# Kernel optimization log

Hardware: AMD Instinct MI355X
Metric: run time of the kernel (lower is better)

## Reference

```python
import jax, jax.numpy as jnp
import numpy as np

B, S, D = 2, 2048, 768
C = 8                # num_channels
R = D // C           # ternary_rank = 96 (RoPE head_dim)
THETA = 10000.0
TERNARY_STD = 0.2
TERNARY_SCALE = 1.0  # ternary_factor_scaling


def _rope_tables():
    # HF-style RoPE: inv_freq over half dim, emb = concat(freqs, freqs)
    inv_freq = 1.0 / (THETA ** (np.arange(0, R, 2, dtype=np.float32) / R))
    pos = np.arange(S, dtype=np.float32)
    freqs = pos[:, None] * inv_freq[None, :]          # [S, R/2]
    emb = np.concatenate([freqs, freqs], axis=-1)     # [S, R]
    cos = np.broadcast_to(np.cos(emb)[None], (B, S, R)).copy()
    sin = np.broadcast_to(np.sin(emb)[None], (B, S, R)).copy()
    return jnp.asarray(cos), jnp.asarray(sin)


def setup_inputs() -> dict:
    key = jax.random.key(0)
    k1, k2, k3 = jax.random.split(key, 3)
    qz = jax.random.normal(k1, (B, S, D), dtype=jnp.float32)
    U = jax.random.normal(k2, (D, D), dtype=jnp.float32) * TERNARY_STD
    V = jax.random.normal(k3, (D, D), dtype=jnp.float32) * TERNARY_STD
    cos, sin = _rope_tables()
    return {"qz": qz, "cos": cos, "sin": sin, "U": U, "V": V}


def _rotate_half(x):
    h = x.shape[-1] // 2
    return jnp.concatenate([-x[..., h:], x[..., :h]], axis=-1)


def reference(qz, cos, sin, U, V):
    # cos/sin: [B,S,R] -> broadcast over channel dim -> [B,1,S,R]
    cosb = cos[:, None, :, :]
    sinb = sin[:, None, :, :]
    rope = lambda x: x * cosb + _rotate_half(x) * sinb       # apply
    rope_o = lambda x: x * cosb - _rotate_half(x) * sinb     # apply_o (inverse)

    # projections: F.linear(qz, W) == qz @ W.T
    qz_u = (qz @ U.T * TERNARY_SCALE).reshape(B, S, C, R).transpose(0, 2, 1, 3)
    qz_v = (qz @ V.T * TERNARY_SCALE).reshape(B, S, C, R).transpose(0, 2, 1, 3)

    qz_uo = rope_o(qz_u)
    qz_ur = rope(qz_u)
    qz_vr = rope(qz_v)

    # message_F: [B,C,S,S]
    message_F = jnp.einsum('bcqr,bckr->bcqk', qz_ur, qz_vr)
    # softmax(message_F / regularize_h) with regularize_h = 1/D  ->  * D
    qh = jax.nn.softmax((message_F * jnp.float32(D)).astype(jnp.float32), axis=-1).astype(qz_ur.dtype)

    qh_v1 = rope_o(jnp.einsum('bcqk,bckr->bcqr', qh, qz_vr))  # qh @ qz_v
    qh_v2 = rope(jnp.einsum('bckq,bckr->bcqr', qh, qz_uo))    # qh^T @ qz_uo

    qh_v1 = qh_v1.transpose(0, 2, 1, 3).reshape(B, S, D)
    qh_v2 = qh_v2.transpose(0, 2, 1, 3).reshape(B, S, D)

    message_G = (qh_v1 @ U + qh_v2 @ V) * TERNARY_SCALE
    return message_G
```

## Files before the change

### kernel.cpp

```cpp
#include <hip/hip_runtime.h>

typedef _Float16 f16;
typedef _Float16 f16x8 __attribute__((ext_vector_type(8)));
typedef _Float16 f16x4 __attribute__((ext_vector_type(4)));
typedef float f32x4 __attribute__((ext_vector_type(4)));

#define MFMA16(A,B,C) __builtin_amdgcn_mfma_f32_16x16x32_f16(A,B,C,0,0,0)
#define INV2048 4.8828125e-4f
#define HN (16ll*2048*96)
#define UVN 589824
#define ZC1 1107.98979f
#define ZC2 0.54101064f

__device__ __forceinline__ void split_f16(float x, f16& h, f16& l) {
    h = (f16)x;
    l = (f16)((x - (float)h) * 2048.0f);
}

__global__ __launch_bounds__(256) void k0_split(const float* __restrict__ qz,
                                                const float* __restrict__ U,
                                                const float* __restrict__ V,
                                                f16* __restrict__ qzh, f16* __restrict__ qzl,
                                                f16* __restrict__ Uh, f16* __restrict__ Ul,
                                                f16* __restrict__ Vh, f16* __restrict__ Vl) {
    const int i4 = blockIdx.x * 256 + threadIdx.x;
    {
        float4 x = *(const float4*)(qz + (size_t)i4 * 4);
        f16 h0, l0, h1, l1, h2, l2, h3, l3;
        split_f16(x.x, h0, l0); split_f16(x.y, h1, l1);
        split_f16(x.z, h2, l2); split_f16(x.w, h3, l3);
        f16x4 hv = {h0, h1, h2, h3};
        f16x4 lv = {l0, l1, l2, l3};
        *(f16x4*)(qzh + (size_t)i4 * 4) = hv;
        *(f16x4*)(qzl + (size_t)i4 * 4) = lv;
    }
    if (i4 < UVN / 4) {
        float4 x = *(const float4*)(U + (size_t)i4 * 4);
        f16 h0, l0, h1, l1, h2, l2, h3, l3;
        split_f16(x.x, h0, l0); split_f16(x.y, h1, l1);
        split_f16(x.z, h2, l2); split_f16(x.w, h3, l3);
        f16x4 hv = {h0, h1, h2, h3};
        f16x4 lv = {l0, l1, l2, l3};
        *(f16x4*)(Uh + (size_t)i4 * 4) = hv;
        *(f16x4*)(Ul + (size_t)i4 * 4) = lv;
        float4 y = *(const float4*)(V + (size_t)i4 * 4);
        split_f16(y.x, h0, l0); split_f16(y.y, h1, l1);
        split_f16(y.z, h2, l2); split_f16(y.w, h3, l3);
        f16x4 hv2 = {h0, h1, h2, h3};
        f16x4 lv2 = {l0, l1, l2, l3};
        *(f16x4*)(Vh + (size_t)i4 * 4) = hv2;
        *(f16x4*)(Vl + (size_t)i4 * 4) = lv2;
    }
}

__global__ __launch_bounds__(256, 2) void k1_proj(const f16* __restrict__ qzh,
                                                  const f16* __restrict__ qzl,
                                                  const f16* __restrict__ Uh,
                                                  const f16* __restrict__ Ul,
                                                  const f16* __restrict__ Vh,
                                                  const f16* __restrict__ Vl,
                                                  const float* __restrict__ cosb,
                                                  const float* __restrict__ sinb,
                                                  f16* __restrict__ uhp, f16* __restrict__ ulp,
                                                  f16* __restrict__ vhp, f16* __restrict__ vlp,
                                                  f16* __restrict__ vT, f16* __restrict__ oT) {
    __shared__ __align__(16) f16 smem[36864];
    f16* sAh  = smem;
    f16* sAl  = smem + 4608;
    f16* sBuh = smem + 9216;
    f16* sBul = smem + 9216 + 6912;
    f16* sBvh = smem + 9216 + 2 * 6912;
    f16* sBvl = smem + 9216 + 3 * 6912;

    const int tid = threadIdx.x;
    const int w = tid >> 6, lane = tid & 63;
    const int quad = lane >> 4, l15 = lane & 15;
    const int wr = w >> 1, wc = w & 1;
    const int bid0 = blockIdx.y * 64 + blockIdx.x;
    const int swz  = (bid0 & 7) * 64 + (bid0 >> 3);
    const int bs0 = (swz & 63) * 64;
    const int c = swz >> 6;

    const f16* Ug_h = Uh + (size_t)c * 96 * 768;
    const f16* Ug_l = Ul + (size_t)c * 96 * 768;
    const f16* Vg_h = Vh + (size_t)c * 96 * 768;
    const f16* Vg_l = Vl + (size_t)c * 96 * 768;

    f32x4 aUS[2][3] = {}, aUX[2][3] = {};
    f32x4 aVS[2][3] = {}, aVX[2][3] = {};

    for (int k0 = 0; k0 < 768; k0 += 64) {
        __syncthreads();
#pragma unroll
        for (int m = 0; m < 2; ++m) {
            int f = tid + 256 * m, row = f >> 3, cg = f & 7;
            const size_t go = (size_t)(bs0 + row) * 768 + k0 + cg * 8;
            const int lo = row * 72 + cg * 8;
            *(float4*)&sAh[lo] = *(const float4*)(qzh + go);
            *(float4*)&sAl[lo] = *(const float4*)(qzl + go);
        }
#pragma unroll
        for (int m = 0; m < 3; ++m) {
            int f = tid + 256 * m, row = f >> 3, cg = f & 7;
            const size_t go = (size_t)row * 768 + k0 + cg * 8;
            const int lo = row * 72 + cg * 8;
            *(float4*)&sBuh[lo] = *(const float4*)(Ug_h + go);
            *(float4*)&sBul[lo] = *(const float4*)(Ug_l + go);
            *(float4*)&sBvh[lo] = *(const float4*)(Vg_h + go);
            *(float4*)&sBvl[lo] = *(const float4*)(Vg_l + go);
        }
        __syncthreads();
#pragma unroll
        for (int cc = 0; cc < 2; ++cc) {
            f16x8 ah[2], al[2];
#pragma unroll
            for (int mt = 0; mt < 2; ++mt) {
                const int ar = (32 * wr + 16 * mt + l15) * 72 + cc * 32 + quad * 8;
                ah[mt] = *(const f16x8*)&sAh[ar];
                al[mt] = *(const f16x8*)&sAl[ar];
            }
#pragma unroll
            for (int nt = 0; nt < 3; ++nt) {
                const int br = (48 * wc + 16 * nt + l15) * 72 + cc * 32 + quad * 8;
                f16x8 buh = *(const f16x8*)&sBuh[br];
                f16x8 bul = *(const f16x8*)&sBul[br];
                f16x8 bvh = *(const f16x8*)&sBvh[br];
                f16x8 bvl = *(const f16x8*)&sBvl[br];
#pragma unroll
                for (int mt = 0; mt < 2; ++mt) {
                    aUS[mt][nt] = MFMA16(ah[mt], buh, aUS[mt][nt]);
                    aUX[mt][nt] = MFMA16(ah[mt], bul, aUX[mt][nt]);
                    aUX[mt][nt] = MFMA16(al[mt], buh, aUX[mt][nt]);
                    aVS[mt][nt] = MFMA16(ah[mt], bvh, aVS[mt][nt]);
                    aVX[mt][nt] = MFMA16(ah[mt], bvl, aVX[mt][nt]);
                    aVX[mt][nt] = MFMA16(al[mt], bvh, aVX[mt][nt]);
                }
            }
        }
    }

    __syncthreads();
    float* LU = (float*)smem;
    float* LV = LU + 6400;
#pragma unroll
    for (int mt = 0; mt < 2; ++mt)
#pragma unroll
        for (int nt = 0; nt < 3; ++nt)
#pragma unroll
            for (int r = 0; r < 4; ++r) {
                const int sl = 32 * wr + 16 * mt + 4 * quad + r;
                const int col = 48 * wc + 16 * nt + l15;
                LU[sl * 100 + col] = aUS[mt][nt][r] + aUX[mt][nt][r] * INV2048;
                LV[sl * 100 + col] = aVS[mt][nt][r] + aVX[mt][nt][r] * INV2048;
            }
    __syncthreads();

    const int b = bs0 >> 11;
    const int s0 = bs0 & 2047;
    const int head = b * 8 + c;
    const size_t nb = (size_t)head * 2048 * 96;
    const size_t tb = (size_t)head * 96 * 2048;
    const int ty = tid >> 4, tx = tid & 15;

#pragma unroll
    for (int jj = 0; jj < 3; ++jj) {
        int r = tx + 16 * jj;
        f16 vt1[4], vt2[4], ot1[4], ot2[4];
#pragma unroll
        for (int ii = 0; ii < 4; ++ii) {
            int sl = 4 * ty + ii;
            int s = s0 + sl;
            int cbi = (b * 2048 + s) * 96 + r;
            float cc = cosb[cbi], ss = sinb[cbi];
            size_t rowb = nb + (size_t)s * 96;
            float u1 = LU[sl * 100 + r], u2 = LU[sl * 100 + r + 48];
            float v1 = LV[sl * 100 + r], v2 = LV[sl * 100 + r + 48];
            float ur1 = u1 * cc - u2 * ss, ur2 = u2 * cc + u1 * ss;
            float uo1 = u1 * cc + u2 * ss, uo2 = u2 * cc - u1 * ss;
            float vr1 = v1 * cc - v2 * ss, vr2 = v2 * cc + v1 * ss;
            f16 h, l;
            split_f16(ur1, h, l); uhp[rowb + r] = h;      ulp[rowb + r] = l;
            split_f16(ur2, h, l); uhp[rowb + r + 48] = h; ulp[rowb + r + 48] = l;
            split_f16(vr1, h, l); vhp[rowb + r] = h;      vlp[rowb + r] = l;      vt1[ii] = h;
            split_f16(vr2, h, l); vhp[rowb + r + 48] = h; vlp[rowb + r + 48] = l; vt2[ii] = h;
            ot1[ii] = (f16)uo1; ot2[ii] = (f16)uo2;
        }
        f16x4 pv1 = {vt1[0], vt1[1], vt1[2], vt1[3]};
        f16x4 pv2 = {vt2[0], vt2[1], vt2[2], vt2[3]};
        f16x4 po1 = {ot1[0], ot1[1], ot1[2], ot1[3]};
        f16x4 po2 = {ot2[0], ot2[1], ot2[2], ot2[3]};
        *(f16x4*)&vT[tb + (size_t)r * 2048 + s0 + 4 * ty] = pv1;
        *(f16x4*)&vT[tb + (size_t)(r + 48) * 2048 + s0 + 4 * ty] = pv2;
        *(f16x4*)&oT[tb + (size_t)r * 2048 + s0 + 4 * ty] = po1;
        *(f16x4*)&oT[tb + (size_t)(r + 48) * 2048 + s0 + 4 * ty] = po2;
    }
}

__global__ __launch_bounds__(256, 2) void k2_stats(const f16* __restrict__ uhp,
                                                   const f16* __restrict__ ulp,
                                                   const f16* __restrict__ vhp,
                                                   const f16* __restrict__ vlp,
                                                   float* __restrict__ Mo) {
    __shared__ float Mbuf[4][64];
    const int tid = threadIdx.x, w = tid >> 6, lane = tid & 63;
    const int quad = lane >> 4, l15 = lane & 15;
    const int bid0 = blockIdx.y * 32 + blockIdx.x;
    const int swz  = (bid0 & 7) * 64 + (bid0 >> 3);
    const int q0 = (swz & 31) * 64, head = swz >> 5;
    const f16* Ah_g = uhp + (size_t)head * 2048 * 96;
    const f16* Al_g = ulp + (size_t)head * 2048 * 96;

    f16x8 Afh[4][3], Afl[4][3];
#pragma unroll
    for (int mt = 0; mt < 4; ++mt)
#pragma unroll
        for (int cc = 0; cc < 3; ++cc) {
            size_t off = (size_t)(q0 + 16 * mt + l15) * 96 + cc * 32 + quad * 8;
            Afh[mt][cc] = *(const f16x8*)(Ah_g + off);
            Afl[mt][cc] = *(const f16x8*)(Al_g + off);
        }

    const f16* Bh_p = vhp + (size_t)head * 2048 * 96 + (size_t)(w * 16 + l15) * 96 + quad * 8;
    const f16* Bl_p = vlp + (size_t)head * 2048 * 96 + (size_t)(w * 16 + l15) * 96 + quad * 8;

    f16x8 Bch[2][3], Bcl[2][3];
#pragma unroll
    for (int cc = 0; cc < 3; ++cc) {
        Bch[0][cc] = *(const f16x8*)(Bh_p + cc * 32);
        Bcl[0][cc] = *(const f16x8*)(Bl_p + cc * 32);
    }

    float m_run[4][4];
#pragma unroll
    for (int mt = 0; mt < 4; ++mt)
#pragma unroll
        for (int r = 0; r < 4; ++r) m_run[mt][r] = -3.0e38f;

    for (int tp = 0; tp < 16; ++tp) {
#pragma unroll
        for (int h = 0; h < 2; ++h) {
            const int t = 2 * tp + h;
            if (t < 31) {
                const f16* bh = Bh_p + (size_t)(t + 1) * 6144;
                const f16* bl = Bl_p + (size_t)(t + 1) * 6144;
#pragma unroll
                for (int cc = 0; cc < 3; ++cc) {
                    Bch[h ^ 1][cc] = *(const f16x8*)(bh + cc * 32);
                    Bcl[h ^ 1][cc] = *(const f16x8*)(bl + cc * 32);
                }
            }
            f32x4 accS[4] = {}, accX[4] = {};
            __builtin_amdgcn_s_setprio(1);
#pragma unroll
            for (int cc = 0; cc < 3; ++cc)
#pragma unroll
                for (int mt = 0; mt < 4; ++mt) {
                    accS[mt] = MFMA16(Afh[mt][cc], Bch[h][cc], accS[mt]);
                    accX[mt] = MFMA16(Afh[mt][cc], Bcl[h][cc], accX[mt]);
                    accX[mt] = MFMA16(Afl[mt][cc], Bch[h][cc], accX[mt]);
                }
            __builtin_amdgcn_s_setprio(0);
#pragma unroll
            for (int mt = 0; mt < 4; ++mt)
#pragma unroll
                for (int r = 0; r < 4; ++r) {
                    float zl = fmaf(ZC1, accS[mt][r], ZC2 * accX[mt][r]);
                    m_run[mt][r] = fmaxf(m_run[mt][r], zl);
                }
        }
    }
#pragma unroll
    for (int mt = 0; mt < 4; ++mt)
#pragma unroll
        for (int r = 0; r < 4; ++r) {
            float m = m_run[mt][r];
            m = fmaxf(m, __shfl_xor(m, 1)); m = fmaxf(m, __shfl_xor(m, 2));
            m = fmaxf(m, __shfl_xor(m, 4)); m = fmaxf(m, __shfl_xor(m, 8));
            m_run[mt][r] = m;
        }
    if (l15 == 0) {
#pragma unroll
        for (int mt = 0; mt < 4; ++mt)
#pragma unroll
            for (int r = 0; r < 4; ++r)
                Mbuf[w][16 * mt + 4 * quad + r] = m_run[mt][r];
    }
    __syncthreads();
    if (tid < 64) {
        float M = -3.0e38f;
#pragma unroll
        for (int ww = 0; ww < 4; ++ww) M = fmaxf(M, Mbuf[ww][tid]);
        Mo[head * 2048 + q0 + tid] = M;
    }
}

__global__ __launch_bounds__(256, 2) void k3a(const f16* __restrict__ uhp,
                                              const f16* __restrict__ ulp,
                                              const f16* __restrict__ vhp,
                                              const f16* __restrict__ vlp,
                                              const f16* __restrict__ vT,
                                              const float* __restrict__ Mo,
                                              float* __restrict__ Lo,
                                              const float* __restrict__ cosb,
                                              const float* __restrict__ sinb,
                                              f16* __restrict__ w1) {
    __shared__ f16 Vt[2][112 * 72];
    __shared__ f16 P[2][64 * 72];
    const int tid = threadIdx.x, w = tid >> 6, lane = tid & 63;
    const int quad = lane >> 4, l15 = lane & 15;
    const int bid0 = blockIdx.y * 32 + blockIdx.x;
    const int swz  = (bid0 & 7) * 64 + (bid0 >> 3);
    const int q0 = (swz & 31) * 64, head = swz >> 5;
    const f16* Ah_g = uhp + (size_t)head * 2048 * 96;
    const f16* Al_g = ulp + (size_t)head * 2048 * 96;
    const f16* Vt_g = vT + (size_t)head * 96 * 2048;

    f16x8 Afh[4][3], Afl[4][3];
#pragma unroll
    for (int mt = 0; mt < 4; ++mt)
#pragma unroll
        for (int cc = 0; cc < 3; ++cc) {
            size_t off = (size_t)(q0 + 16 * mt + l15) * 96 + cc * 32 + quad * 8;
            Afh[mt][cc] = *(const f16x8*)(Ah_g + off);
            Afl[mt][cc] = *(const f16x8*)(Al_g + off);
        }
    float negM[4][4];
#pragma unroll
    for (int mt = 0; mt < 4; ++mt)
#pragma unroll
        for (int r = 0; r < 4; ++r)
            negM[mt][r] = -Mo[head * 2048 + q0 + 16 * mt + 4 * quad + r];

    const f16* Bh_p = vhp + (size_t)head * 2048 * 96 + (size_t)(w * 16 + l15) * 96 + quad * 8;
    const f16* Bl_p = vlp + (size_t)head * 2048 * 96 + (size_t)(w * 16 + l15) * 96 + quad * 8;
    const int vr0 = tid >> 3, vc8 = (tid & 7) * 8;
    const int pwc = (w * 16 + l15 + 16 * quad) & 63;
    const int prr = 16 * (l15 >> 2);

    if (tid < 144) {
        f16x8 ones = {(f16)1, (f16)1, (f16)1, (f16)1,
                      (f16)1, (f16)1, (f16)1, (f16)1};
        *(f16x8*)&Vt[0][96 * 72 + tid * 8] = ones;
        *(f16x8*)&Vt[1][96 * 72 + tid * 8] = ones;
    }

    f16x8 Bch[2][3], Bcl[2][3];
    float4 v0, v1, v2;
#pragma unroll
    for (int cc = 0; cc < 3; ++cc) {
        Bch[0][cc] = *(const f16x8*)(Bh_p + cc * 32);
        Bcl[0][cc] = *(const f16x8*)(Bl_p + cc * 32);
    }
    v0 = *(const float4*)(Vt_g + (size_t)vr0 * 2048 + vc8);
    v1 = *(const float4*)(Vt_g + (size_t)(vr0 + 32) * 2048 + vc8);
    v2 = *(const float4*)(Vt_g + (size_t)(vr0 + 64) * 2048 + vc8);
    *(float4*)&Vt[0][vr0 * 72 + vc8] = v0;
    *(float4*)&Vt[0][(vr0 + 32) * 72 + vc8] = v1;
    *(float4*)&Vt[0][(vr0 + 64) * 72 + vc8] = v2;

    f32x4 accO[7] = {};

    for (int tp = 0; tp < 16; ++tp) {
#pragma unroll
        for (int h = 0; h < 2; ++h) {
            const int t = 2 * tp + h;
            if (t < 31) {
                const f16* bh = Bh_p + (size_t)(t + 1) * 6144;
                const f16* bl = Bl_p + (size_t)(t + 1) * 6144;
                const int kn = (t + 1) * 64;
#pragma unroll
                for (int cc = 0; cc < 3; ++cc) {
                    Bch[h ^ 1][cc] = *(const f16x8*)(bh + cc * 32);
                    Bcl[h ^ 1][cc] = *(const f16x8*)(bl + cc * 32);
                }
                v0 = *(const float4*)(Vt_g + (size_t)vr0 * 2048 + kn + vc8);
                v1 = *(const float4*)(Vt_g + (size_t)(vr0 + 32) * 2048 + kn + vc8);
                v2 = *(const float4*)(Vt_g + (size_t)(vr0 + 64) * 2048 + kn + vc8);
            }
            f32x4 accS[4] = {}, accX[4] = {};
            __builtin_amdgcn_s_setprio(1);
#pragma unroll
            for (int cc = 0; cc < 3; ++cc)
#pragma unroll
                for (int mt = 0; mt < 4; ++mt) {
                    accS[mt] = MFMA16(Afh[mt][cc], Bch[h][cc], accS[mt]);
                    accX[mt] = MFMA16(Afh[mt][cc], Bcl[h][cc], accX[mt]);
                    accX[mt] = MFMA16(Afl[mt][cc], Bch[h][cc], accX[mt]);
                }
            __builtin_amdgcn_s_setprio(0);
#pragma unroll
            for (int mt = 0; mt < 4; ++mt)
#pragma unroll
                for (int r = 0; r < 4; ++r) {
                    float zl = fmaf(ZC1, accS[mt][r], ZC2 * accX[mt][r]);
                    P[h][(16 * mt + 4 * quad + r) * 72 + pwc] =
                        (f16)exp2f(zl + negM[mt][r]);
                }
            __syncthreads();
            __builtin_amdgcn_s_setprio(1);
#pragma unroll
            for (int kc = 0; kc < 2; ++kc) {
                f16x8 ap = *(const f16x8*)&P[h][(w * 16 + l15) * 72 +
                                               ((kc * 32 + quad * 8 + prr) & 63)];
#pragma unroll
                for (int nt = 0; nt < 7; ++nt) {
                    f16x8 bv = *(const f16x8*)&Vt[h][(nt * 16 + l15) * 72 + kc * 32 + quad * 8];
                    accO[nt] = MFMA16(ap, bv, accO[nt]);
                }
            }
            __builtin_amdgcn_s_setprio(0);
            if (t < 31) {
                *(float4*)&Vt[h ^ 1][vr0 * 72 + vc8] = v0;
                *(float4*)&Vt[h ^ 1][(vr0 + 32) * 72 + vc8] = v1;
                *(float4*)&Vt[h ^ 1][(vr0 + 64) * 72 + vc8] = v2;
            }
        }
    }
    float invL[4];
#pragma unroll
    for (int r = 0; r < 4; ++r) invL[r] = 1.0f / accO[6][r];
    if (l15 == 0) {
#pragma unroll
        for (int r = 0; r < 4; ++r)
            Lo[head * 2048 + q0 + w * 16 + quad * 4 + r] = accO[6][r];
    }

    const int b = head >> 3, c = head & 7;
#pragma unroll
    for (int r = 0; r < 4; ++r) {
        int q = q0 + w * 16 + quad * 4 + r;
        int cbi = (b * 2048 + q) * 96;
        f16* wrow = w1 + (size_t)(b * 2048 + q) * 768 + c * 96;
#pragma unroll
        for (int nt = 0; nt < 3; ++nt) {
            int rr = nt * 16 + l15;
            float cc = cosb[cbi + rr], ss = sinb[cbi + rr];
            float a = accO[nt][r] * invL[r];
            float b2 = accO[nt + 3][r] * invL[r];
            wrow[rr] = (f16)(a * cc + b2 * ss);
            wrow[rr + 48] = (f16)(b2 * cc - a * ss);
        }
    }
}

__global__ __launch_bounds__(256, 2) void k3b(const f16* __restrict__ uhp,
                                              const f16* __restrict__ ulp,
                                              const f16* __restrict__ vhp,
                                              const f16* __restrict__ vlp,
                                              const f16* __restrict__ oT,
                                              const float* __restrict__ Mo,
                                              const float* __restrict__ Lo,
                                              const float* __restrict__ cosb,
                                              const float* __restrict__ sinb,
                                              f16* __restrict__ w2) {
    __shared__ f16 Ot[2][96 * 72];
    __shared__ f16 P[2][64 * 72];
    const int tid = threadIdx.x, w = tid >> 6, lane = tid & 63;
    const int quad = lane >> 4, l15 = lane & 15;
    const int bid0 = blockIdx.y * 32 + blockIdx.x;
    const int swz  = (bid0 & 7) * 64 + (bid0 >> 3);
    const int q0 = (swz & 31) * 64, head = swz >> 5;
    const f16* Ah_g = vhp + (size_t)head * 2048 * 96;
    const f16* Al_g = vlp + (size_t)head * 2048 * 96;
    const f16* Ot_g = oT + (size_t)head * 96 * 2048;

    f16x8 Afh[4][3], Afl[4][3];
#pragma unroll
    for (int mt = 0; mt < 4; ++mt)
#pragma unroll
        for (int cc = 0; cc < 3; ++cc) {
            size_t off = (size_t)(q0 + 16 * mt + l15) * 96 + cc * 32 + quad * 8;
            Afh[mt][cc] = *(const f16x8*)(Ah_g + off);
            Afl[mt][cc] = *(const f16x8*)(Al_g + off);
        }

    const f16* Bh_p = uhp + (size_t)head * 2048 * 96 + (size_t)(w * 16 + l15) * 96 + quad * 8;
    const f16* Bl_p = ulp + (size_t)head * 2048 * 96 + (size_t)(w * 16 + l15) * 96 + quad * 8;
    const int vr0 = tid >> 3, vc8 = (tid & 7) * 8;
    const int pwc = (w * 16 + l15 + 16 * quad) & 63;
    const int prr = 16 * (l15 >> 2);

    f16x8 Bch[2][3], Bcl[2][3];
    float4 v0, v1, v2;
#pragma unroll
    for (int cc = 0; cc < 3; ++cc) {
        Bch[0][cc] = *(const f16x8*)(Bh_p + cc * 32);
        Bcl[0][cc] = *(const f16x8*)(Bl_p + cc * 32);
    }
    v0 = *(const float4*)(Ot_g + (size_t)vr0 * 2048 + vc8);
    v1 = *(const float4*)(Ot_g + (size_t)(vr0 + 32) * 2048 + vc8);
    v2 = *(const float4*)(Ot_g + (size_t)(vr0 + 64) * 2048 + vc8);
    *(float4*)&Ot[0][vr0 * 72 + vc8] = v0;
    *(float4*)&Ot[0][(vr0 + 32) * 72 + vc8] = v1;
    *(float4*)&Ot[0][(vr0 + 64) * 72 + vc8] = v2;

    f32x4 accO[6] = {};

    for (int tp = 0; tp < 16; ++tp) {
#pragma unroll
        for (int h = 0; h < 2; ++h) {
            const int t = 2 * tp + h;
            const int k0 = t * 64;
            float negMk = -Mo[head * 2048 + k0 + w * 16 + l15];
            float invLk = 1.0f / Lo[head * 2048 + k0 + w * 16 + l15];
            if (t < 31) {
                const f16* bh = Bh_p + (size_t)(t + 1) * 6144;
                const f16* bl = Bl_p + (size_t)(t + 1) * 6144;
                const int kn = (t + 1) * 64;
#pragma unroll
                for (int cc = 0; cc < 3; ++cc) {
                    Bch[h ^ 1][cc] = *(const f16x8*)(bh + cc * 32);
                    Bcl[h ^ 1][cc] = *(const f16x8*)(bl + cc * 32);
                }
                v0 = *(const float4*)(Ot_g + (size_t)vr0 * 2048 + kn + vc8);
                v1 = *(const float4*)(Ot_g + (size_t)(vr0 + 32) * 2048 + kn + vc8);
                v2 = *(const float4*)(Ot_g + (size_t)(vr0 + 64) * 2048 + kn + vc8);
            }
            f32x4 accS[4] = {}, accX[4] = {};
            __builtin_amdgcn_s_setprio(1);
#pragma unroll
            for (int cc = 0; cc < 3; ++cc)
#pragma unroll
                for (int mt = 0; mt < 4; ++mt) {
                    accS[mt] = MFMA16(Afh[mt][cc], Bch[h][cc], accS[mt]);
                    accX[mt] = MFMA16(Afl[mt][cc], Bch[h][cc], accX[mt]);
                    accX[mt] = MFMA16(Afh[mt][cc], Bcl[h][cc], accX[mt]);
                }
            __builtin_amdgcn_s_setprio(0);
#pragma unroll
            for (int mt = 0; mt < 4; ++mt)
#pragma unroll
                for (int r = 0; r < 4; ++r) {
                    float zl = fmaf(ZC1, accS[mt][r], ZC2 * accX[mt][r]);
                    P[h][(16 * mt + 4 * quad + r) * 72 + pwc] =
                        (f16)(exp2f(zl + negMk) * invLk);
                }
            __syncthreads();
            __builtin_amdgcn_s_setprio(1);
#pragma unroll
            for (int kc = 0; kc < 2; ++kc) {
                f16x8 ap = *(const f16x8*)&P[h][(w * 16 + l15) * 72 +
                                               ((kc * 32 + quad * 8 + prr) & 63)];
#pragma unroll
                for (int nt = 0; nt < 6; ++nt) {
                    f16x8 bo = *(const f16x8*)&Ot[h][(nt * 16 + l15) * 72 + kc * 32 + quad * 8];
                    accO[nt] = MFMA16(ap, bo, accO[nt]);
                }
            }
            __builtin_amdgcn_s_setprio(0);
            if (t < 31) {
                *(float4*)&Ot[h ^ 1][vr0 * 72 + vc8] = v0;
                *(float4*)&Ot[h ^ 1][(vr0 + 32) * 72 + vc8] = v1;
                *(float4*)&Ot[h ^ 1][(vr0 + 64) * 72 + vc8] = v2;
            }
        }
    }
    const int b = head >> 3, c = head & 7;
#pragma unroll
    for (int r = 0; r < 4; ++r) {
        int q = q0 + w * 16 + quad * 4 + r;
        int cbi = (b * 2048 + q) * 96;
        f16* wrow = w2 + (size_t)(b * 2048 + q) * 768 + c * 96;
#pragma unroll
        for (int nt = 0; nt < 3; ++nt) {
            int rr = nt * 16 + l15;
            float cc = cosb[cbi + rr], ss = sinb[cbi + rr];
            float a = accO[nt][r];
            float b2 = accO[nt + 3][r];
            wrow[rr] = (f16)(a * cc - b2 * ss);
            wrow[rr + 48] = (f16)(b2 * cc + a * ss);
        }
    }
}

__global__ __launch_bounds__(256, 2) void k4_final(const f16* __restrict__ w1,
                                                   const f16* __restrict__ w2,
                                                   const float* __restrict__ U,
                                                   const float* __restrict__ V,
                                                   float* __restrict__ outp) {
    __shared__ f16 A1[128 * 56];
    __shared__ f16 A2[128 * 56];
    __shared__ f16 B1[64 * 56];
    __shared__ f16 B2[64 * 56];
    const int tid = threadIdx.x, w = tid >> 6, lane = tid & 63;
    const int quad = lane >> 4, l15 = lane & 15;
    const int bs0 = blockIdx.x * 128;
    const int d0 = blockIdx.y * 64;
    f32x4 acc[2][4] = {};

    for (int ec = 0; ec < 24; ++ec) {
        int e0 = ec * 32;
        __syncthreads();
#pragma unroll
        for (int m = 0; m < 2; ++m) {
            int f = tid + 256 * m;
            int row = f >> 2, q = f & 3;
            *(float4*)&A1[row * 56 + q * 8] =
                *(const float4*)(w1 + (size_t)(bs0 + row) * 768 + e0 + q * 8);
            *(float4*)&A2[row * 56 + q * 8] =
                *(const float4*)(w2 + (size_t)(bs0 + row) * 768 + e0 + q * 8);
        }
#pragma unroll
        for (int m2 = 0; m2 < 2; ++m2) {
            int e_r = (tid >> 4) + 16 * m2;
            int dc = tid & 15;
            float4 fu = *(const float4*)(U + (size_t)(e0 + e_r) * 768 + d0 + dc * 4);
            float4 fv = *(const float4*)(V + (size_t)(e0 + e_r) * 768 + d0 + dc * 4);
            B1[(dc * 4 + 0) * 56 + e_r] = (f16)fu.x;
            B1[(dc * 4 + 1) * 56 + e_r] = (f16)fu.y;
            B1[(dc * 4 + 2) * 56 + e_r] = (f16)fu.z;
            B1[(dc * 4 + 3) * 56 + e_r] = (f16)fu.w;
            B2[(dc * 4 + 0) * 56 + e_r] = (f16)fv.x;
            B2[(dc * 4 + 1) * 56 + e_r] = (f16)fv.y;
            B2[(dc * 4 + 2) * 56 + e_r] = (f16)fv.z;
            B2[(dc * 4 + 3) * 56 + e_r] = (f16)fv.w;
        }
        __syncthreads();
        f16x8 a1f[2], a2f[2];
#pragma unroll
        for (int mt = 0; mt < 2; ++mt) {
            a1f[mt] = *(const f16x8*)&A1[(32 * w + 16 * mt + l15) * 56 + quad * 8];
            a2f[mt] = *(const f16x8*)&A2[(32 * w + 16 * mt + l15) * 56 + quad * 8];
        }
#pragma unroll
        for (int nt = 0; nt < 4; ++nt) {
            f16x8 b1f = *(const f16x8*)&B1[(nt * 16 + l15) * 56 + quad * 8];
            f16x8 b2f = *(const f16x8*)&B2[(nt * 16 + l15) * 56 + quad * 8];
#pragma unroll
            for (int mt = 0; mt < 2; ++mt) {
                acc[mt][nt] = MFMA16(a1f[mt], b1f, acc[mt][nt]);
                acc[mt][nt] = MFMA16(a2f[mt], b2f, acc[mt][nt]);
            }
        }
    }
#pragma unroll
    for (int mt = 0; mt < 2; ++mt)
#pragma unroll
        for (int nt = 0; nt < 4; ++nt)
#pragma unroll
            for (int r = 0; r < 4; ++r) {
                int s = bs0 + 32 * w + 16 * mt + 4 * quad + r;
                int d = d0 + 16 * nt + l15;
                outp[(size_t)s * 768 + d] = acc[mt][nt][r];
            }
}

extern "C" void kernel_launch(void* const* d_in, const int* in_sizes, int n_in,
                              void* d_out, int out_size, void* d_ws, size_t ws_size,
                              hipStream_t stream) {
    const float* qz   = (const float*)d_in[0];
    const float* cosb = (const float*)d_in[1];
    const float* sinb = (const float*)d_in[2];
    const float* U    = (const float*)d_in[3];
    const float* V    = (const float*)d_in[4];
    float* outp = (float*)d_out;

    f16* ws16 = (f16*)d_ws;
    f16* uhp = ws16;
    f16* ulp = ws16 + HN;
    f16* vhp = ws16 + 2 * HN;
    f16* vlp = ws16 + 3 * HN;
    f16* vT  = ws16 + 4 * HN;
    f16* oT  = ws16 + 5 * HN;
    f16* w1  = ws16 + 6 * HN;
    f16* w2  = ws16 + 7 * HN;
    float* Mo = (float*)(ws16 + 8 * HN);
    float* Lo = Mo + 16 * 2048;

    f16* qzh = w1;
    f16* qzl = w2;
    f16* outw = (f16*)d_out;
    f16* Uh = outw;
    f16* Ul = outw + UVN;
    f16* Vh = outw + 2 * UVN;
    f16* Vl = outw + 3 * UVN;

    k0_split<<<dim3(3072), 256, 0, stream>>>(qz, U, V, qzh, qzl, Uh, Ul, Vh, Vl);
    k1_proj<<<dim3(64, 8), 256, 0, stream>>>(qzh, qzl, Uh, Ul, Vh, Vl, cosb, sinb,
                                             uhp, ulp, vhp, vlp, vT, oT);
    k2_stats<<<dim3(32, 16), 256, 0, stream>>>(uhp, ulp, vhp, vlp, Mo);
    k3a<<<dim3(32, 16), 256, 0, stream>>>(uhp, ulp, vhp, vlp, vT, Mo, Lo, cosb, sinb, w1);
    k3b<<<dim3(32, 16), 256, 0, stream>>>(uhp, ulp, vhp, vlp, oT, Mo, Lo, cosb, sinb, w2);
    k4_final<<<dim3(32, 12), 256, 0, stream>>>(w1, w2, U, V, outp);
}
```

Measured before the change: 326.3 us.

## Halve query tile per block and split PV output columns across wave pairs

```diff
diff --git a/kernel.cpp b/kernel.cpp
--- a/kernel.cpp
+++ b/kernel.cpp
@@ -196,23 +196,23 @@
     }
 }
 
-__global__ __launch_bounds__(256, 2) void k2_stats(const f16* __restrict__ uhp,
+__global__ __launch_bounds__(256, 3) void k2_stats(const f16* __restrict__ uhp,
                                                    const f16* __restrict__ ulp,
                                                    const f16* __restrict__ vhp,
                                                    const f16* __restrict__ vlp,
                                                    float* __restrict__ Mo) {
-    __shared__ float Mbuf[4][64];
+    __shared__ float Mbuf[4][32];
     const int tid = threadIdx.x, w = tid >> 6, lane = tid & 63;
     const int quad = lane >> 4, l15 = lane & 15;
-    const int bid0 = blockIdx.y * 32 + blockIdx.x;
-    const int swz  = (bid0 & 7) * 64 + (bid0 >> 3);
-    const int q0 = (swz & 31) * 64, head = swz >> 5;
+    const int bid0 = blockIdx.y * 64 + blockIdx.x;
+    const int swz  = (bid0 & 7) * 128 + (bid0 >> 3);
+    const int q0 = (swz & 63) * 32, head = swz >> 6;
     const f16* Ah_g = uhp + (size_t)head * 2048 * 96;
     const f16* Al_g = ulp + (size_t)head * 2048 * 96;
 
-    f16x8 Afh[4][3], Afl[4][3];
-#pragma unroll
-    for (int mt = 0; mt < 4; ++mt)
+    f16x8 Afh[2][3], Afl[2][3];
+#pragma unroll
+    for (int mt = 0; mt < 2; ++mt)
 #pragma unroll
         for (int cc = 0; cc < 3; ++cc) {
             size_t off = (size_t)(q0 + 16 * mt + l15) * 96 + cc * 32 + quad * 8;
@@ -230,9 +230,9 @@
         Bcl[0][cc] = *(const f16x8*)(Bl_p + cc * 32);
     }
 
-    float m_run[4][4];
-#pragma unroll
-    for (int mt = 0; mt < 4; ++mt)
+    float m_run[2][4];
+#pragma unroll
+    for (int mt = 0; mt < 2; ++mt)
 #pragma unroll
         for (int r = 0; r < 4; ++r) m_run[mt][r] = -3.0e38f;
 
@@ -249,19 +249,19 @@
                     Bcl[h ^ 1][cc] = *(const f16x8*)(bl + cc * 32);
                 }
             }
-            f32x4 accS[4] = {}, accX[4] = {};
+            f32x4 accS[2] = {}, accX[2] = {};
             __builtin_amdgcn_s_setprio(1);
 #pragma unroll
             for (int cc = 0; cc < 3; ++cc)
 #pragma unroll
-                for (int mt = 0; mt < 4; ++mt) {
+                for (int mt = 0; mt < 2; ++mt) {
                     accS[mt] = MFMA16(Afh[mt][cc], Bch[h][cc], accS[mt]);
                     accX[mt] = MFMA16(Afh[mt][cc], Bcl[h][cc], accX[mt]);
                     accX[mt] = MFMA16(Afl[mt][cc], Bch[h][cc], accX[mt]);
                 }
             __builtin_amdgcn_s_setprio(0);
 #pragma unroll
-            for (int mt = 0; mt < 4; ++mt)
+            for (int mt = 0; mt < 2; ++mt)
 #pragma unroll
                 for (int r = 0; r < 4; ++r) {
                     float zl = fmaf(ZC1, accS[mt][r], ZC2 * accX[mt][r]);
@@ -270,7 +270,7 @@
         }
     }
 #pragma unroll
-    for (int mt = 0; mt < 4; ++mt)
+    for (int mt = 0; mt < 2; ++mt)
 #pragma unroll
         for (int r = 0; r < 4; ++r) {
             float m = m_run[mt][r];
@@ -280,13 +280,13 @@
         }
     if (l15 == 0) {
 #pragma unroll
-        for (int mt = 0; mt < 4; ++mt)
+        for (int mt = 0; mt < 2; ++mt)
 #pragma unroll
             for (int r = 0; r < 4; ++r)
                 Mbuf[w][16 * mt + 4 * quad + r] = m_run[mt][r];
     }
     __syncthreads();
-    if (tid < 64) {
+    if (tid < 32) {
         float M = -3.0e38f;
 #pragma unroll
         for (int ww = 0; ww < 4; ++ww) M = fmaxf(M, Mbuf[ww][tid]);
@@ -294,7 +294,7 @@
     }
 }
 
-__global__ __launch_bounds__(256, 2) void k3a(const f16* __restrict__ uhp,
+__global__ __launch_bounds__(256, 3) void k3a(const f16* __restrict__ uhp,
                                               const f16* __restrict__ ulp,
                                               const f16* __restrict__ vhp,
                                               const f16* __restrict__ vlp,
@@ -305,28 +305,30 @@
                                               const float* __restrict__ sinb,
                                               f16* __restrict__ w1) {
     __shared__ f16 Vt[2][112 * 72];
-    __shared__ f16 P[2][64 * 72];
+    __shared__ f16 P[2][32 * 72];
+    __shared__ float Lbuf[32];
     const int tid = threadIdx.x, w = tid >> 6, lane = tid & 63;
     const int quad = lane >> 4, l15 = lane & 15;
-    const int bid0 = blockIdx.y * 32 + blockIdx.x;
-    const int swz  = (bid0 & 7) * 64 + (bid0 >> 3);
-    const int q0 = (swz & 31) * 64, head = swz >> 5;
+    const int qg = w & 1;
+    const int bid0 = blockIdx.y * 64 + blockIdx.x;
+    const int swz  = (bid0 & 7) * 128 + (bid0 >> 3);
+    const int q0 = (swz & 63) * 32, head = swz >> 6;
     const f16* Ah_g = uhp + (size_t)head * 2048 * 96;
     const f16* Al_g = ulp + (size_t)head * 2048 * 96;
     const f16* Vt_g = vT + (size_t)head * 96 * 2048;
 
-    f16x8 Afh[4][3], Afl[4][3];
-#pragma unroll
-    for (int mt = 0; mt < 4; ++mt)
+    f16x8 Afh[2][3], Afl[2][3];
+#pragma unroll
+    for (int mt = 0; mt < 2; ++mt)
 #pragma unroll
         for (int cc = 0; cc < 3; ++cc) {
             size_t off = (size_t)(q0 + 16 * mt + l15) * 96 + cc * 32 + quad * 8;
             Afh[mt][cc] = *(const f16x8*)(Ah_g + off);
             Afl[mt][cc] = *(const f16x8*)(Al_g + off);
         }
-    float negM[4][4];
-#pragma unroll
-    for (int mt = 0; mt < 4; ++mt)
+    float negM[2][4];
+#pragma unroll
+    for (int mt = 0; mt < 2; ++mt)
 #pragma unroll
         for (int r = 0; r < 4; ++r)
             negM[mt][r] = -Mo[head * 2048 + q0 + 16 * mt + 4 * quad + r];
@@ -358,7 +360,7 @@
     *(float4*)&Vt[0][(vr0 + 32) * 72 + vc8] = v1;
     *(float4*)&Vt[0][(vr0 + 64) * 72 + vc8] = v2;
 
-    f32x4 accO[7] = {};
+    f32x4 accO[4] = {};
 
     for (int tp = 0; tp < 16; ++tp) {
 #pragma unroll
@@ -377,19 +379,19 @@
                 v1 = *(const float4*)(Vt_g + (size_t)(vr0 + 32) * 2048 + kn + vc8);
                 v2 = *(const float4*)(Vt_g + (size_t)(vr0 + 64) * 2048 + kn + vc8);
             }
-            f32x4 accS[4] = {}, accX[4] = {};
+            f32x4 accS[2] = {}, accX[2] = {};
             __builtin_amdgcn_s_setprio(1);
 #pragma unroll
             for (int cc = 0; cc < 3; ++cc)
 #pragma unroll
-                for (int mt = 0; mt < 4; ++mt) {
+                for (int mt = 0; mt < 2; ++mt) {
                     accS[mt] = MFMA16(Afh[mt][cc], Bch[h][cc], accS[mt]);
                     accX[mt] = MFMA16(Afh[mt][cc], Bcl[h][cc], accX[mt]);
                     accX[mt] = MFMA16(Afl[mt][cc], Bch[h][cc], accX[mt]);
                 }
             __builtin_amdgcn_s_setprio(0);
 #pragma unroll
-            for (int mt = 0; mt < 4; ++mt)
+            for (int mt = 0; mt < 2; ++mt)
 #pragma unroll
                 for (int r = 0; r < 4; ++r) {
                     float zl = fmaf(ZC1, accS[mt][r], ZC2 * accX[mt][r]);
@@ -400,12 +402,22 @@
             __builtin_amdgcn_s_setprio(1);
 #pragma unroll
             for (int kc = 0; kc < 2; ++kc) {
-                f16x8 ap = *(const f16x8*)&P[h][(w * 16 + l15) * 72 +
+                f16x8 ap = *(const f16x8*)&P[h][(qg * 16 + l15) * 72 +
                                                ((kc * 32 + quad * 8 + prr) & 63)];
-#pragma unroll
-                for (int nt = 0; nt < 7; ++nt) {
-                    f16x8 bv = *(const f16x8*)&Vt[h][(nt * 16 + l15) * 72 + kc * 32 + quad * 8];
-                    accO[nt] = MFMA16(ap, bv, accO[nt]);
+                if (w < 2) {
+                    const int nts[4] = {0, 1, 3, 4};
+#pragma unroll
+                    for (int j = 0; j < 4; ++j) {
+                        f16x8 bv = *(const f16x8*)&Vt[h][(nts[j] * 16 + l15) * 72 + kc * 32 + quad * 8];
+                        accO[j] = MFMA16(ap, bv, accO[j]);
+                    }
+                } else {
+                    const int nts[3] = {2, 5, 6};
+#pragma unroll
+                    for (int j = 0; j < 3; ++j) {
+                        f16x8 bv = *(const f16x8*)&Vt[h][(nts[j] * 16 + l15) * 72 + kc * 32 + quad * 8];
+                        accO[j] = MFMA16(ap, bv, accO[j]);
+                    }
                 }
             }
             __builtin_amdgcn_s_setprio(0);
@@ -416,34 +428,46 @@
             }
         }
     }
+    if (w >= 2 && l15 == 0) {
+#pragma unroll
+        for (int r = 0; r < 4; ++r) {
+            Lbuf[qg * 16 + 4 * quad + r] = accO[2][r];
+            Lo[head * 2048 + q0 + qg * 16 + 4 * quad + r] = accO[2][r];
+        }
+    }
+    __syncthreads();
     float invL[4];
 #pragma unroll
-    for (int r = 0; r < 4; ++r) invL[r] = 1.0f / accO[6][r];
-    if (l15 == 0) {
-#pragma unroll
-        for (int r = 0; r < 4; ++r)
-            Lo[head * 2048 + q0 + w * 16 + quad * 4 + r] = accO[6][r];
-    }
+    for (int r = 0; r < 4; ++r) invL[r] = 1.0f / Lbuf[qg * 16 + 4 * quad + r];
 
     const int b = head >> 3, c = head & 7;
 #pragma unroll
     for (int r = 0; r < 4; ++r) {
-        int q = q0 + w * 16 + quad * 4 + r;
+        int q = q0 + qg * 16 + quad * 4 + r;
         int cbi = (b * 2048 + q) * 96;
         f16* wrow = w1 + (size_t)(b * 2048 + q) * 768 + c * 96;
-#pragma unroll
-        for (int nt = 0; nt < 3; ++nt) {
-            int rr = nt * 16 + l15;
+        if (w < 2) {
+#pragma unroll
+            for (int p = 0; p < 2; ++p) {
+                int rr = p * 16 + l15;
+                float cc = cosb[cbi + rr], ss = sinb[cbi + rr];
+                float a = accO[p][r] * invL[r];
+                float b2 = accO[p + 2][r] * invL[r];
+                wrow[rr] = (f16)(a * cc + b2 * ss);
+                wrow[rr + 48] = (f16)(b2 * cc - a * ss);
+            }
+        } else {
+            int rr = 32 + l15;
             float cc = cosb[cbi + rr], ss = sinb[cbi + rr];
-            float a = accO[nt][r] * invL[r];
-            float b2 = accO[nt + 3][r] * invL[r];
+            float a = accO[0][r] * invL[r];
+            float b2 = accO[1][r] * invL[r];
             wrow[rr] = (f16)(a * cc + b2 * ss);
             wrow[rr + 48] = (f16)(b2 * cc - a * ss);
         }
     }
 }
 
-__global__ __launch_bounds__(256, 2) void k3b(const f16* __restrict__ uhp,
+__global__ __launch_bounds__(256, 3) void k3b(const f16* __restrict__ uhp,
                                               const f16* __restrict__ ulp,
                                               const f16* __restrict__ vhp,
                                               const f16* __restrict__ vlp,
@@ -454,19 +478,20 @@
                                               const float* __restrict__ sinb,
                                               f16* __restrict__ w2) {
     __shared__ f16 Ot[2][96 * 72];
-    __shared__ f16 P[2][64 * 72];
+    __shared__ f16 P[2][32 * 72];
     const int tid = threadIdx.x, w = tid >> 6, lane = tid & 63;
     const int quad = lane >> 4, l15 = lane & 15;
-    const int bid0 = blockIdx.y * 32 + blockIdx.x;
-    const int swz  = (bid0 & 7) * 64 + (bid0 >> 3);
-    const int q0 = (swz & 31) * 64, head = swz >> 5;
+    const int qg = w & 1;
+    const int bid0 = blockIdx.y * 64 + blockIdx.x;
+    const int swz  = (bid0 & 7) * 128 + (bid0 >> 3);
+    const int q0 = (swz & 63) * 32, head = swz >> 6;
     const f16* Ah_g = vhp + (size_t)head * 2048 * 96;
     const f16* Al_g = vlp + (size_t)head * 2048 * 96;
     const f16* Ot_g = oT + (size_t)head * 96 * 2048;
 
-    f16x8 Afh[4][3], Afl[4][3];
-#pragma unroll
-    for (int mt = 0; mt < 4; ++mt)
+    f16x8 Afh[2][3], Afl[2][3];
+#pragma unroll
+    for (int mt = 0; mt < 2; ++mt)
 #pragma unroll
         for (int cc = 0; cc < 3; ++cc) {
             size_t off = (size_t)(q0 + 16 * mt + l15) * 96 + cc * 32 + quad * 8;
@@ -494,7 +519,7 @@
     *(float4*)&Ot[0][(vr0 + 32) * 72 + vc8] = v1;
     *(float4*)&Ot[0][(vr0 + 64) * 72 + vc8] = v2;
 
-    f32x4 accO[6] = {};
+    f32x4 accO[4] = {};
 
     for (int tp = 0; tp < 16; ++tp) {
 #pragma unroll
@@ -516,19 +541,19 @@
                 v1 = *(const float4*)(Ot_g + (size_t)(vr0 + 32) * 2048 + kn + vc8);
                 v2 = *(const float4*)(Ot_g + (size_t)(vr0 + 64) * 2048 + kn + vc8);
             }
-            f32x4 accS[4] = {}, accX[4] = {};
+            f32x4 accS[2] = {}, accX[2] = {};
             __builtin_amdgcn_s_setprio(1);
 #pragma unroll
             for (int cc = 0; cc < 3; ++cc)
 #pragma unroll
-                for (int mt = 0; mt < 4; ++mt) {
+                for (int mt = 0; mt < 2; ++mt) {
                     accS[mt] = MFMA16(Afh[mt][cc], Bch[h][cc], accS[mt]);
                     accX[mt] = MFMA16(Afl[mt][cc], Bch[h][cc], accX[mt]);
                     accX[mt] = MFMA16(Afh[mt][cc], Bcl[h][cc], accX[mt]);
                 }
             __builtin_amdgcn_s_setprio(0);
 #pragma unroll
-            for (int mt = 0; mt < 4; ++mt)
+            for (int mt = 0; mt < 2; ++mt)
 #pragma unroll
                 for (int r = 0; r < 4; ++r) {
                     float zl = fmaf(ZC1, accS[mt][r], ZC2 * accX[mt][r]);
@@ -539,12 +564,22 @@
             __builtin_amdgcn_s_setprio(1);
 #pragma unroll
             for (int kc = 0; kc < 2; ++kc) {
-                f16x8 ap = *(const f16x8*)&P[h][(w * 16 + l15) * 72 +
+                f16x8 ap = *(const f16x8*)&P[h][(qg * 16 + l15) * 72 +
                                                ((kc * 32 + quad * 8 + prr) & 63)];
-#pragma unroll
-                for (int nt = 0; nt < 6; ++nt) {
-                    f16x8 bo = *(const f16x8*)&Ot[h][(nt * 16 + l15) * 72 + kc * 32 + quad * 8];
-                    accO[nt] = MFMA16(ap, bo, accO[nt]);
+                if (w < 2) {
+                    const int nts[4] = {0, 1, 3, 4};
+#pragma unroll
+                    for (int j = 0; j < 4; ++j) {
+                        f16x8 bo = *(const f16x8*)&Ot[h][(nts[j] * 16 + l15) * 72 + kc * 32 + quad * 8];
+                        accO[j] = MFMA16(ap, bo, accO[j]);
+                    }
+                } else {
+                    const int nts[2] = {2, 5};
+#pragma unroll
+                    for (int j = 0; j < 2; ++j) {
+                        f16x8 bo = *(const f16x8*)&Ot[h][(nts[j] * 16 + l15) * 72 + kc * 32 + quad * 8];
+                        accO[j] = MFMA16(ap, bo, accO[j]);
+                    }
                 }
             }
             __builtin_amdgcn_s_setprio(0);
@@ -558,15 +593,24 @@
     const int b = head >> 3, c = head & 7;
 #pragma unroll
     for (int r = 0; r < 4; ++r) {
-        int q = q0 + w * 16 + quad * 4 + r;
+        int q = q0 + qg * 16 + quad * 4 + r;
         int cbi = (b * 2048 + q) * 96;
         f16* wrow = w2 + (size_t)(b * 2048 + q) * 768 + c * 96;
-#pragma unroll
-        for (int nt = 0; nt < 3; ++nt) {
-            int rr = nt * 16 + l15;
+        if (w < 2) {
+#pragma unroll
+            for (int p = 0; p < 2; ++p) {
+                int rr = p * 16 + l15;
+                float cc = cosb[cbi + rr], ss = sinb[cbi + rr];
+                float a = accO[p][r];
+                float b2 = accO[p + 2][r];
+                wrow[rr] = (f16)(a * cc - b2 * ss);
+                wrow[rr + 48] = (f16)(b2 * cc + a * ss);
+            }
+        } else {
+            int rr = 32 + l15;
             float cc = cosb[cbi + rr], ss = sinb[cbi + rr];
-            float a = accO[nt][r];
-            float b2 = accO[nt + 3][r];
+            float a = accO[0][r];
+            float b2 = accO[1][r];
             wrow[rr] = (f16)(a * cc - b2 * ss);
             wrow[rr + 48] = (f16)(b2 * cc + a * ss);
         }
@@ -584,8 +628,10 @@
     __shared__ f16 B2[64 * 56];
     const int tid = threadIdx.x, w = tid >> 6, lane = tid & 63;
     const int quad = lane >> 4, l15 = lane & 15;
-    const int bs0 = blockIdx.x * 128;
-    const int d0 = blockIdx.y * 64;
+    const int id = blockIdx.y * 32 + blockIdx.x;
+    const int g  = (id & 7) * 48 + (id >> 3);
+    const int bs0 = (g & 31) * 128;
+    const int d0 = (g >> 5) * 64;
     f32x4 acc[2][4] = {};
 
     for (int ec = 0; ec < 24; ++ec) {
@@ -678,8 +724,8 @@
     k0_split<<<dim3(3072), 256, 0, stream>>>(qz, U, V, qzh, qzl, Uh, Ul, Vh, Vl);
     k1_proj<<<dim3(64, 8), 256, 0, stream>>>(qzh, qzl, Uh, Ul, Vh, Vl, cosb, sinb,
                                              uhp, ulp, vhp, vlp, vT, oT);
-    k2_stats<<<dim3(32, 16), 256, 0, stream>>>(uhp, ulp, vhp, vlp, Mo);
-    k3a<<<dim3(32, 16), 256, 0, stream>>>(uhp, ulp, vhp, vlp, vT, Mo, Lo, cosb, sinb, w1);
-    k3b<<<dim3(32, 16), 256, 0, stream>>>(uhp, ulp, vhp, vlp, oT, Mo, Lo, cosb, sinb, w2);
+    k2_stats<<<dim3(64, 16), 256, 0, stream>>>(uhp, ulp, vhp, vlp, Mo);
+    k3a<<<dim3(64, 16), 256, 0, stream>>>(uhp, ulp, vhp, vlp, vT, Mo, Lo, cosb, sinb, w1);
+    k3b<<<dim3(64, 16), 256, 0, stream>>>(uhp, ulp, vhp, vlp, oT, Mo, Lo, cosb, sinb, w2);
     k4_final<<<dim3(32, 12), 256, 0, stream>>>(w1, w2, U, V, outp);
 }
```

New measurement: 428.2 us. 1.31x slower.
